# Kernel optimization log

Hardware: AMD Instinct MI355X
Metric: run time of the kernel (lower is better)

The kernel has to match this reference:

```python
import jax, jax.numpy as jnp
import numpy as np

D_MODEL, SEQ, D_HEAD, N_HEAD, D_MLP = 1024, 2048, 64, 16, 4096
BATCH = 2
LN_EPS = 1e-5


def layer_norm(x, gamma, beta):
    mu = jnp.mean(x, axis=-1, keepdims=True)
    var = jnp.mean(jnp.square(x - mu), axis=-1, keepdims=True)
    return (x - mu) * jax.lax.rsqrt(var + LN_EPS) * gamma + beta


def setup_inputs() -> dict:
    key = jax.random.key(0)
    ks = jax.random.split(key, 10)
    s = 1.0 / np.sqrt(D_MODEL)
    x = jax.random.normal(ks[0], (BATCH, SEQ, D_MODEL), dtype=jnp.float32)
    # per-head Q/K/V projections, stacked: [H, d_model, d_head]
    wq = jax.random.uniform(ks[1], (N_HEAD, D_MODEL, D_HEAD), jnp.float32, -s, s)
    wk = jax.random.uniform(ks[2], (N_HEAD, D_MODEL, D_HEAD), jnp.float32, -s, s)
    wv = jax.random.uniform(ks[3], (N_HEAD, D_MODEL, D_HEAD), jnp.float32, -s, s)
    wo = jax.random.uniform(ks[4], (N_HEAD * D_HEAD, D_MODEL), jnp.float32, -s, s)
    sm = 1.0 / np.sqrt(D_MLP)
    w_in = jax.random.uniform(ks[5], (D_MODEL, D_MLP), jnp.float32, -s, s)
    b_in = jax.random.uniform(ks[6], (D_MLP,), jnp.float32, -s, s)
    w_out = jax.random.uniform(ks[7], (D_MLP, D_MODEL), jnp.float32, -sm, sm)
    b_out = jax.random.uniform(ks[8], (D_MODEL,), jnp.float32, -sm, sm)
    g1 = jnp.ones((D_MODEL,), jnp.float32)
    bt1 = jnp.zeros((D_MODEL,), jnp.float32)
    g2 = jnp.ones((D_MODEL,), jnp.float32)
    bt2 = jnp.zeros((D_MODEL,), jnp.float32)
    return {"x": x, "wq": wq, "wk": wk, "wv": wv, "wo": wo,
            "w_in": w_in, "b_in": b_in, "w_out": w_out, "b_out": b_out,
            "g1": g1, "bt1": bt1, "g2": g2, "bt2": bt2}


def reference(x, wq, wk, wv, wo, w_in, b_in, w_out, b_out, g1, bt1, g2, bt2):
    B, S, D = x.shape
    # multi-head attention (all heads batched)
    q = jnp.einsum('bsd,hde->bhse', x, wq)  # [B,H,S,dh]
    k = jnp.einsum('bsd,hde->bhse', x, wk)
    v = jnp.einsum('bsd,hde->bhse', x, wv)
    scores = jnp.einsum('bhie,bhje->bhij', q, k) / np.sqrt(D_HEAD)
    causal = jnp.tril(jnp.ones((S, S), dtype=bool))
    scores = jnp.where(causal, scores, -jnp.inf)
    attn = jax.nn.softmax(scores, axis=-1)
    head_out = jnp.einsum('bhij,bhje->bhie', attn, v)  # [B,H,S,dh]
    # concat heads in order (head 0 first) -> [B,S,H*dh]
    head_out = jnp.transpose(head_out, (0, 2, 1, 3)).reshape(B, S, N_HEAD * D_HEAD)
    x = x + layer_norm(head_out @ wo, g1, bt1)
    mlp = jax.nn.relu(x @ w_in + b_in) @ w_out + b_out
    x = x + layer_norm(mlp, g2, bt2)
    return x
```

## Files before the change

### kernel.cpp

```cpp
#include <hip/hip_runtime.h>
#include <hip/hip_bf16.h>
#include <math.h>

#define DM 1024
#define SEQ 2048
#define DH 64
#define NH 16
#define DMLP 4096
#define BATCH 2
#define ROWS (BATCH*SEQ)

typedef __attribute__((ext_vector_type(4))) float f32x4;
typedef __attribute__((ext_vector_type(8))) short bf16x8;

__device__ __forceinline__ void gl2lds16(const __hip_bfloat16* g, __hip_bfloat16* l) {
  __builtin_amdgcn_global_load_lds(
      (const __attribute__((address_space(1))) void*)g,
      (__attribute__((address_space(3))) void*)l, 16, 0, 0);
}

template<int K, int OUT_BF16, int BIAS, int RELU>
__global__ __launch_bounds__(512) void gemm256(
    const __hip_bfloat16* __restrict__ A,
    const __hip_bfloat16* __restrict__ BT,
    float* __restrict__ Cf,
    __hip_bfloat16* __restrict__ Cb,
    const float* __restrict__ bias,
    int N)
{
  constexpr int NT = K / 64;
  __shared__ __align__(16) __hip_bfloat16 As[2][16384];
  __shared__ __align__(16) __hip_bfloat16 Bs[2][16384];
  const int t    = threadIdx.x;
  const int wave = t >> 6;
  const int lane = t & 63;
  const int col  = lane & 15;
  const int quad = lane >> 4;
  const int m0 = blockIdx.x * 256;
  const int n0 = blockIdx.y * 256;
  const int wm = (wave >> 2) * 128;
  const int wn = (wave & 3) * 64;

  const int tr = t >> 3;
  const int tc = (t & 7) ^ (tr & 7);
  const __hip_bfloat16* gA = A  + (size_t)(m0 + tr) * K + tc * 8;
  const __hip_bfloat16* gB = BT + (size_t)(n0 + tr) * K + tc * 8;

  const int sw  = col & 7;
  const int ao0 = ((quad)     ^ sw) * 8;
  const int ao1 = ((4 + quad) ^ sw) * 8;

  f32x4 acc[8][4] = {};

#define STAGE_A(h, u) do {                                                     \
    gl2lds16(gA + (size_t)(h)*128*K + (u)*64,                                  \
             &As[(u)&1][(h)*8192 + wave*512]);                                 \
    gl2lds16(gA + (size_t)(h)*128*K + (u)*64 + (size_t)64*K,                   \
             &As[(u)&1][(h)*8192 + 4096 + wave*512]);                          \
  } while (0)
#define STAGE_B(h, u) do {                                                     \
    gl2lds16(gB + (size_t)(h)*128*K + (u)*64,                                  \
             &Bs[(u)&1][(h)*8192 + wave*512]);                                 \
    gl2lds16(gB + (size_t)(h)*128*K + (u)*64 + (size_t)64*K,                   \
             &Bs[(u)&1][(h)*8192 + 4096 + wave*512]);                          \
  } while (0)
#define LOAD_A(base) do { _Pragma("unroll")                                    \
    for (int i = 0; i < 4; ++i) {                                              \
      af[i][0] = *(const bf16x8*)(pA + (base) + i*1024 + ao0);                 \
      af[i][1] = *(const bf16x8*)(pA + (base) + i*1024 + ao1);                 \
    } } while (0)
#define LOAD_BX(arr, base) do { _Pragma("unroll")                              \
    for (int j = 0; j < 2; ++j) {                                              \
      arr[j][0] = *(const bf16x8*)(pB + (base) + j*1024 + ao0);                \
      arr[j][1] = *(const bf16x8*)(pB + (base) + j*1024 + ao1);                \
    } } while (0)
#define PHASE_TAIL(MB, NB, BARR) do {                                          \
    asm volatile("s_barrier" ::: "memory");                                    \
    asm volatile("s_waitcnt lgkmcnt(0)" ::: "memory");                         \
    __builtin_amdgcn_s_setprio(1);                                             \
    _Pragma("unroll")                                                          \
    for (int kk = 0; kk < 2; ++kk)                                             \
      _Pragma("unroll")                                                        \
      for (int i = 0; i < 4; ++i)                                              \
        _Pragma("unroll")                                                      \
        for (int j = 0; j < 2; ++j)                                            \
          acc[(MB)+i][(NB)+j] = __builtin_amdgcn_mfma_f32_16x16x32_bf16(       \
              af[i][kk], BARR[j][kk], acc[(MB)+i][(NB)+j], 0, 0, 0);           \
    __builtin_amdgcn_s_setprio(0);                                             \
    asm volatile("s_barrier" ::: "memory");                                    \
  } while (0)

  STAGE_A(0, 0); STAGE_B(0, 0); STAGE_A(1, 0); STAGE_B(1, 0);
  if (NT > 1) {
    STAGE_A(0, 1); STAGE_B(0, 1); STAGE_A(1, 1); STAGE_B(1, 1);
    asm volatile("s_waitcnt vmcnt(8)" ::: "memory");
  } else {
    asm volatile("s_waitcnt vmcnt(0)" ::: "memory");
  }
  asm volatile("s_barrier" ::: "memory");

  #pragma unroll 2
  for (int u = 0; u < NT; ++u) {
    const __hip_bfloat16* pA = As[u & 1] + (wm + col) * 64;
    const __hip_bfloat16* pB = Bs[u & 1] + (wn + col) * 64;
    const bool s2 = (u + 2 < NT);
    bf16x8 af[4][2], bl[2][2], bh[2][2];

    LOAD_A(0);
    LOAD_BX(bl, 0);
    PHASE_TAIL(0, 0, bl);

    LOAD_BX(bh, 2048);
    PHASE_TAIL(0, 2, bh);

    LOAD_A(4096);
    if (s2) { STAGE_B(0, u + 2); STAGE_B(1, u + 2); }
    PHASE_TAIL(4, 2, bh);

    if (s2) {
      STAGE_A(0, u + 2); STAGE_A(1, u + 2);
      asm volatile("s_waitcnt vmcnt(8)" ::: "memory");
    } else {
      asm volatile("s_waitcnt vmcnt(0)" ::: "memory");
    }
    PHASE_TAIL(4, 0, bl);
  }
#undef STAGE_A
#undef STAGE_B
#undef LOAD_A
#undef LOAD_BX
#undef PHASE_TAIL

  #pragma unroll
  for (int mi = 0; mi < 8; ++mi) {
    #pragma unroll
    for (int ni = 0; ni < 4; ++ni) {
      const int cn = n0 + wn + ni*16 + col;
      float bv = 0.f;
      if (BIAS) bv = bias[cn];
      #pragma unroll
      for (int r = 0; r < 4; ++r) {
        const int cm = m0 + wm + mi*16 + quad*4 + r;
        float v = acc[mi][ni][r];
        if (BIAS) v += bv;
        if (RELU) v = fmaxf(v, 0.f);
        if (OUT_BF16) Cb[(size_t)cm * N + cn] = __float2bfloat16(v);
        else          Cf[(size_t)cm * N + cn] = v;
      }
    }
  }
}

template<int TM, int SPLIT, int OUT_BF16, int BIAS, int RELU>
__global__ __launch_bounds__(256) void gemm_bt(
    const __hip_bfloat16* __restrict__ A,
    const __hip_bfloat16* __restrict__ BT,
    float* __restrict__ Cf,
    __hip_bfloat16* __restrict__ Cb,
    const float* __restrict__ bias,
    int M, int N, int K, long long zstride)
{
  constexpr int ASZ = TM*32;
  constexpr int MI  = (TM == 128) ? 4 : 2;
  __shared__ __align__(16) __hip_bfloat16 As[2*ASZ];
  __shared__ __align__(16) __hip_bfloat16 Bs[2*4096];
  const int t    = threadIdx.x;
  const int wave = t >> 6;
  const int lane = t & 63;
  const int col  = lane & 15;
  const int quad = lane >> 4;
  const int m0 = blockIdx.x * TM;
  const int n0 = blockIdx.y * 128;
  const int wm = (wave >> 1) * (TM/2);
  const int wn = (wave & 1) * 64;

  const int Ks = K / SPLIT;
  const int kz = (SPLIT > 1) ? (int)blockIdx.z * Ks : 0;

  const int srow = t >> 2;
  const int scw  = ((t & 3) ^ ((srow >> 1) & 3)) * 8;
  const __hip_bfloat16* gA = A  + (size_t)(m0 + srow) * K + kz + scw;
  const __hip_bfloat16* gB = BT + (size_t)(n0 + srow) * K + kz + scw;
  const size_t rstep = (size_t)64 * K;

  const int scr = (quad ^ ((col >> 1) & 3)) * 8;

  f32x4 acc[MI][4] = {};

#define ISSUE(k0, buf) do {                                            \
    __hip_bfloat16* la = As + (buf)*ASZ  + wave*512;                   \
    __hip_bfloat16* lb = Bs + (buf)*4096 + wave*512;                   \
    gl2lds16(gA + (k0), la);                                           \
    if (TM == 128) gl2lds16(gA + rstep + (k0), la + 2048);             \
    gl2lds16(gB + (k0), lb);                                           \
    gl2lds16(gB + rstep + (k0), lb + 2048);                            \
  } while (0)

  ISSUE(0, 0);
  for (int k0 = 0; k0 < Ks; k0 += 32) {
    const int cur = (k0 >> 5) & 1;
    __syncthreads();
    if (k0 + 32 < Ks) ISSUE(k0 + 32, cur ^ 1);
    const __hip_bfloat16* Ab = As + cur*ASZ;
    const __hip_bfloat16* Bb = Bs + cur*4096;
    bf16x8 af[MI], bf[4];
    #pragma unroll
    for (int i = 0; i < MI; i++)
      af[i] = *(const bf16x8*)&Ab[(wm + i*16 + col)*32 + scr];
    #pragma unroll
    for (int j = 0; j < 4; j++)
      bf[j] = *(const bf16x8*)&Bb[(wn + j*16 + col)*32 + scr];
    #pragma unroll
    for (int i = 0; i < MI; i++)
      #pragma unroll
      for (int j = 0; j < 4; j++)
        acc[i][j] = __builtin_amdgcn_mfma_f32_16x16x32_bf16(af[i], bf[j], acc[i][j], 0, 0, 0);
  }
#undef ISSUE

  float* Cfz = (SPLIT > 1) ? (Cf + (size_t)blockIdx.z * zstride) : Cf;

  #pragma unroll
  for (int i = 0; i < MI; i++) {
    #pragma unroll
    for (int j = 0; j < 4; j++) {
      const int cn = n0 + wn + j*16 + col;
      float bv = 0.f;
      if (BIAS) bv = bias[cn];
      #pragma unroll
      for (int r = 0; r < 4; r++) {
        const int cm = m0 + wm + i*16 + quad*4 + r;
        float v = acc[i][j][r];
        if (BIAS) v += bv;
        if (RELU) v = fmaxf(v, 0.f);
        if (OUT_BF16) Cb[(size_t)cm * N + cn] = __float2bfloat16(v);
        else          Cfz[(size_t)cm * N + cn] = v;
      }
    }
  }
}

__global__ __launch_bounds__(256) void attn_kernel(
    const __hip_bfloat16* __restrict__ qkv,
    const __hip_bfloat16* __restrict__ vt,
    __hip_bfloat16* __restrict__ aout)
{
  __shared__ __align__(16) __hip_bfloat16 Ks[2][64*64];
  __shared__ __align__(16) __hip_bfloat16 Vts[2][64*64];
  __shared__ __align__(16) __hip_bfloat16 Ps[4][16*64];

  const int bh = blockIdx.x, b = bh >> 4, h = bh & 15;
  const int t = threadIdx.x, wave = t >> 6, lane = t & 63;
  const int col = lane & 15, quad = lane >> 4;
  const float SC = 0.125f * 1.44269504f;

  const int r0  = t >> 3;
  const int cs0 = (t & 7) ^ (r0 & 7);
  const __hip_bfloat16* kbase = qkv + (size_t)b*SEQ*3072 + 1024 + h*64;
  const __hip_bfloat16* vbase = vt + (size_t)bh*64*SEQ;

#define AISSUE(j0, buf) do {                                                      \
    gl2lds16(kbase + (size_t)((j0) + r0)*3072      + cs0*8, &Ks[buf][wave*512]);  \
    gl2lds16(kbase + (size_t)((j0) + 32 + r0)*3072 + cs0*8, &Ks[buf][2048 + wave*512]); \
    gl2lds16(vbase + (size_t)r0*SEQ        + (j0) + cs0*8,  &Vts[buf][wave*512]); \
    gl2lds16(vbase + (size_t)(32 + r0)*SEQ + (j0) + cs0*8,  &Vts[buf][2048 + wave*512]); \
  } while (0)

  #pragma unroll 1
  for (int half = 0; half < 2; half++) {
    const int tile = half ? (31 - (int)blockIdx.y) : (int)blockIdx.y;
    const int i0 = tile * 64;
    const int i0w = i0 + wave*16;

    bf16x8 aq[2];
    #pragma unroll
    for (int kk = 0; kk < 2; kk++)
      aq[kk] = *(const bf16x8*)&qkv[((size_t)(b*SEQ + i0w + col))*3072 + h*64 + kk*32 + quad*8];

    f32x4 O[4] = {};
    float lsum[4] = {0.f, 0.f, 0.f, 0.f};

    const int njt = tile + 1;
    __syncthreads();
    AISSUE(0, 0);
    for (int jt = 0; jt < njt; jt++) {
      const int cur = jt & 1;
      const int j0 = jt * 64;
      __syncthreads();
      if (jt + 1 < njt) AISSUE(j0 + 64, cur ^ 1);

      f32x4 S[4] = {};
      #pragma unroll
      for (int kk = 0; kk < 2; kk++) {
        const int sl = ((kk*4 + quad) ^ (col & 7)) * 8;
        #pragma unroll
        for (int jl = 0; jl < 4; jl++) {
          bf16x8 bk = *(const bf16x8*)&Ks[cur][(jl*16 + col)*64 + sl];
          S[jl] = __builtin_amdgcn_mfma_f32_16x16x32_bf16(aq[kk], bk, S[jl], 0, 0, 0);
        }
      }

      const bool diag = (jt == tile);
      #pragma unroll
      for (int r = 0; r < 4; r++) {
        const int row = quad*4 + r;
        const int ig = i0 + wave*16 + row;
        #pragma unroll
        for (int jl = 0; jl < 4; jl++) {
          float p = exp2f(S[jl][r] * SC);
          if (diag && (j0 + jl*16 + col > ig)) p = 0.f;
          lsum[r] += p;
          const int c = jl*2 + (col >> 3);
          Ps[wave][row*64 + (c ^ (row & 7))*8 + (col & 7)] = __float2bfloat16(p);
        }
      }

      #pragma unroll
      for (int kk = 0; kk < 2; kk++) {
        const int sl = ((kk*4 + quad) ^ (col & 7)) * 8;
        bf16x8 ap = *(const bf16x8*)&Ps[wave][col*64 + sl];
        #pragma unroll
        for (int et = 0; et < 4; et++) {
          bf16x8 bv = *(const bf16x8*)&Vts[cur][(et*16 + col)*64 + sl];
          O[et] = __builtin_amdgcn_mfma_f32_16x16x32_bf16(ap, bv, O[et], 0, 0, 0);
        }
      }
    }

    #pragma unroll
    for (int r = 0; r < 4; r++) {
      float s = lsum[r];
      s += __shfl_xor(s, 1);
      s += __shfl_xor(s, 2);
      s += __shfl_xor(s, 4);
      s += __shfl_xor(s, 8);
      const float inv = 1.f / s;
      const int m = b*SEQ + i0w + quad*4 + r;
      #pragma unroll
      for (int et = 0; et < 4; et++)
        aout[(size_t)m*DM + h*64 + et*16 + col] = __float2bfloat16(O[et][r] * inv);
    }
  }
#undef AISSUE
}

__global__ __launch_bounds__(256) void ln_res(
    const float* __restrict__ y0,
    const float* __restrict__ y1,
    const float* __restrict__ bias,
    const float* __restrict__ xres,
    float* __restrict__ xout,
    __hip_bfloat16* __restrict__ bout,
    const float* __restrict__ gamma,
    const float* __restrict__ beta)
{
  const int row = blockIdx.x;
  const int t = threadIdx.x;
  float4 v = ((const float4*)(y0 + (size_t)row*DM))[t];
  if (y1) {
    const float4 w = ((const float4*)(y1 + (size_t)row*DM))[t];
    v.x += w.x; v.y += w.y; v.z += w.z; v.w += w.w;
  }
  if (bias) {
    const float4 w = ((const float4*)bias)[t];
    v.x += w.x; v.y += w.y; v.z += w.z; v.w += w.w;
  }
  float s  = v.x + v.y + v.z + v.w;
  float sq = v.x*v.x + v.y*v.y + v.z*v.z + v.w*v.w;
  #pragma unroll
  for (int off = 32; off > 0; off >>= 1) {
    s  += __shfl_down(s, off);
    sq += __shfl_down(sq, off);
  }
  __shared__ float red[8];
  const int wave = t >> 6, lane = t & 63;
  if (lane == 0) { red[wave] = s; red[4 + wave] = sq; }
  __syncthreads();
  s  = red[0] + red[1] + red[2] + red[3];
  sq = red[4] + red[5] + red[6] + red[7];
  const float mu   = s * (1.f/DM);
  const float var  = sq * (1.f/DM) - mu*mu;
  const float rstd = rsqrtf(var + 1e-5f);
  const float4 g  = ((const float4*)gamma)[t];
  const float4 bt = ((const float4*)beta)[t];
  const float4 xr = ((const float4*)(xres + (size_t)row*DM))[t];
  float4 o;
  o.x = (v.x - mu)*rstd*g.x + bt.x + xr.x;
  o.y = (v.y - mu)*rstd*g.y + bt.y + xr.y;
  o.z = (v.z - mu)*rstd*g.z + bt.z + xr.z;
  o.w = (v.w - mu)*rstd*g.w + bt.w + xr.w;
  ((float4*)(xout + (size_t)row*DM))[t] = o;
  if (bout) {
    __hip_bfloat16* bp = bout + (size_t)row*DM + t*4;
    bp[0] = __float2bfloat16(o.x);
    bp[1] = __float2bfloat16(o.y);
    bp[2] = __float2bfloat16(o.z);
    bp[3] = __float2bfloat16(o.w);
  }
}

__global__ __launch_bounds__(256) void transpose_cvt(
    const float* __restrict__ src, __hip_bfloat16* __restrict__ dst,
    int K, int N, long long sz, long long dz)
{
  __shared__ float tile[32][33];
  const int z = blockIdx.z;
  const int k0 = blockIdx.y * 32, n0 = blockIdx.x * 32;
  const int tx = threadIdx.x & 31, ty = threadIdx.x >> 5;
  const float* s = src + (size_t)z*sz;
  __hip_bfloat16* d = dst + (size_t)z*dz;
  for (int i = ty; i < 32; i += 8)
    tile[i][tx] = s[(size_t)(k0+i)*N + n0 + tx];
  __syncthreads();
  for (int i = ty; i < 32; i += 8)
    d[(size_t)(n0+i)*K + k0 + tx] = __float2bfloat16(tile[tx][i]);
}

__global__ __launch_bounds__(256) void transpose_v(
    const __hip_bfloat16* __restrict__ qkv, __hip_bfloat16* __restrict__ vt)
{
  __shared__ __hip_bfloat16 tile[32][33];
  const int bh = blockIdx.z, b = bh >> 4, h = bh & 15;
  const int s0 = blockIdx.x * 32, e0 = blockIdx.y * 32;
  const int tx = threadIdx.x & 31, ty = threadIdx.x >> 5;
  for (int i = ty; i < 32; i += 8)
    tile[i][tx] = qkv[(size_t)(b*SEQ + s0+i)*3072 + 2048 + h*64 + e0 + tx];
  __syncthreads();
  for (int i = ty; i < 32; i += 8)
    vt[((size_t)bh*64 + e0+i)*SEQ + s0 + tx] = tile[tx][i];
}

__global__ __launch_bounds__(256) void cvt_bf16(
    const float* __restrict__ src, __hip_bfloat16* __restrict__ dst, int n4)
{
  const int i = blockIdx.x*256 + threadIdx.x;
  if (i < n4) {
    const float4 v = ((const float4*)src)[i];
    dst[i*4+0] = __float2bfloat16(v.x);
    dst[i*4+1] = __float2bfloat16(v.y);
    dst[i*4+2] = __float2bfloat16(v.z);
    dst[i*4+3] = __float2bfloat16(v.w);
  }
}

extern "C" void kernel_launch(void* const* d_in, const int* in_sizes, int n_in,
                              void* d_out, int out_size, void* d_ws, size_t ws_size,
                              hipStream_t stream)
{
  const float* x     = (const float*)d_in[0];
  const float* wq    = (const float*)d_in[1];
  const float* wk    = (const float*)d_in[2];
  const float* wv    = (const float*)d_in[3];
  const float* wo    = (const float*)d_in[4];
  const float* w_in  = (const float*)d_in[5];
  const float* b_in  = (const float*)d_in[6];
  const float* w_out = (const float*)d_in[7];
  const float* b_out = (const float*)d_in[8];
  const float* g1    = (const float*)d_in[9];
  const float* bt1   = (const float*)d_in[10];
  const float* g2    = (const float*)d_in[11];
  const float* bt2   = (const float*)d_in[12];
  float* out = (float*)d_out;

  char* ws = (char*)d_ws;
  __hip_bfloat16* xb     = (__hip_bfloat16*)(ws + 0);
  __hip_bfloat16* wqkvT  = (__hip_bfloat16*)(ws + 8388608);
  __hip_bfloat16* woT    = (__hip_bfloat16*)(ws + 14680064);
  __hip_bfloat16* w_inT  = (__hip_bfloat16*)(ws + 16777216);
  __hip_bfloat16* w_outT = (__hip_bfloat16*)(ws + 25165824);
  __hip_bfloat16* qkvb   = (__hip_bfloat16*)(ws + 33554432);
  __hip_bfloat16* vtb    = (__hip_bfloat16*)(ws + 58720256);
  __hip_bfloat16* attn_o = (__hip_bfloat16*)(ws + 67108864);
  float*          P0     = (float*)(ws + 33554432);
  float*          x1     = (float*)(ws + 75497472);
  __hip_bfloat16* x1b    = (__hip_bfloat16*)(ws + 92274688);
  __hip_bfloat16* hbuf   = (__hip_bfloat16*)(ws + 33554432);
  float*          M0     = (float*)(ws + 0);
  float*          M1     = (float*)(ws + 100663296);
  float*          P1     = (float*)(ws + 50331648);

  const long long PROJ_ZS = (long long)ROWS * DM;
  const long long MLP_ZS  = 100663296LL / 4;

  cvt_bf16<<<ROWS*DM/4/256, 256, 0, stream>>>(x, xb, ROWS*DM/4);

  transpose_cvt<<<dim3(2,32,16), 256, 0, stream>>>(wq, wqkvT,             DM, DH, (long long)DM*DH, (long long)DH*DM);
  transpose_cvt<<<dim3(2,32,16), 256, 0, stream>>>(wk, wqkvT + 1024*1024, DM, DH, (long long)DM*DH, (long long)DH*DM);
  transpose_cvt<<<dim3(2,32,16), 256, 0, stream>>>(wv, wqkvT + 2048*1024, DM, DH, (long long)DM*DH, (long long)DH*DM);
  transpose_cvt<<<dim3(32,32,1),  256, 0, stream>>>(wo,    woT,    DM,   DM,   0, 0);
  transpose_cvt<<<dim3(128,32,1), 256, 0, stream>>>(w_in,  w_inT,  DM,   DMLP, 0, 0);
  transpose_cvt<<<dim3(32,128,1), 256, 0, stream>>>(w_out, w_outT, DMLP, DM,   0, 0);

  gemm256<DM,1,0,0><<<dim3(ROWS/256, 3072/256), 512, 0, stream>>>(xb, wqkvT, nullptr, qkvb, nullptr, 3072);
  transpose_v<<<dim3(SEQ/32, 2, BATCH*NH), 256, 0, stream>>>(qkvb, vtb);
  attn_kernel<<<dim3(BATCH*NH, 16), 256, 0, stream>>>(qkvb, vtb, attn_o);
  gemm_bt<64,2,0,0,0><<<dim3(ROWS/64, DM/128, 2), 256, 0, stream>>>(attn_o, woT, P0, nullptr, nullptr, ROWS, DM, DM, PROJ_ZS);
  ln_res<<<ROWS, 256, 0, stream>>>(P0, P1, nullptr, x, x1, x1b, g1, bt1);
  gemm256<DM,1,1,1><<<dim3(ROWS/256, DMLP/256), 512, 0, stream>>>(x1b, w_inT, nullptr, hbuf, b_in, DMLP);
  gemm_bt<64,2,0,0,0><<<dim3(ROWS/64, DM/128, 2), 256, 0, stream>>>(hbuf, w_outT, M0, nullptr, nullptr, ROWS, DM, DMLP, MLP_ZS);
  ln_res<<<ROWS, 256, 0, stream>>>(M0, M1, b_out, x1, out, nullptr, g2, bt2);
}
```

Before: 255.5 us.

## Replace split-K 64x128 GEMM with 256x128 pipelined 512-thread GEMM for projections

Swaps the gemm_bt kernel used for the attention output projection and the MLP down projection for a new 256x128-tile, 8-wave kernel with 64-wide K tiles. It interleaves global-to-LDS loads with MFMA work using explicit waitcnt/barrier control and setprio. The aim is more operand reuse per LDS load and better overlap of memory with compute. The cost is fewer blocks (256 instead of 1024 per launch), so occupancy and load balance across the CUs may suffer.

```diff
diff --git a/kernel.cpp b/kernel.cpp
--- a/kernel.cpp
+++ b/kernel.cpp
@@ -151,90 +151,120 @@
   }
 }
 
-template<int TM, int SPLIT, int OUT_BF16, int BIAS, int RELU>
-__global__ __launch_bounds__(256) void gemm_bt(
+template<int KS>
+__global__ __launch_bounds__(512) void gemm256x128(
     const __hip_bfloat16* __restrict__ A,
     const __hip_bfloat16* __restrict__ BT,
     float* __restrict__ Cf,
-    __hip_bfloat16* __restrict__ Cb,
-    const float* __restrict__ bias,
-    int M, int N, int K, long long zstride)
-{
-  constexpr int ASZ = TM*32;
-  constexpr int MI  = (TM == 128) ? 4 : 2;
-  __shared__ __align__(16) __hip_bfloat16 As[2*ASZ];
-  __shared__ __align__(16) __hip_bfloat16 Bs[2*4096];
+    int N, int K, long long zstride)
+{
+  constexpr int NT = KS / 64;
+  static_assert(NT >= 2, "pipeline needs >=2 K-tiles");
+  __shared__ __align__(16) __hip_bfloat16 As[2][16384];
+  __shared__ __align__(16) __hip_bfloat16 Bs[2][8192];
   const int t    = threadIdx.x;
   const int wave = t >> 6;
   const int lane = t & 63;
   const int col  = lane & 15;
   const int quad = lane >> 4;
-  const int m0 = blockIdx.x * TM;
+  const int m0 = blockIdx.x * 256;
   const int n0 = blockIdx.y * 128;
-  const int wm = (wave >> 1) * (TM/2);
+  const int kz = (int)blockIdx.z * KS;
+  const int wm = (wave >> 1) * 64;
   const int wn = (wave & 1) * 64;
 
-  const int Ks = K / SPLIT;
-  const int kz = (SPLIT > 1) ? (int)blockIdx.z * Ks : 0;
-
-  const int srow = t >> 2;
-  const int scw  = ((t & 3) ^ ((srow >> 1) & 3)) * 8;
-  const __hip_bfloat16* gA = A  + (size_t)(m0 + srow) * K + kz + scw;
-  const __hip_bfloat16* gB = BT + (size_t)(n0 + srow) * K + kz + scw;
-  const size_t rstep = (size_t)64 * K;
-
-  const int scr = (quad ^ ((col >> 1) & 3)) * 8;
-
-  f32x4 acc[MI][4] = {};
-
-#define ISSUE(k0, buf) do {                                            \
-    __hip_bfloat16* la = As + (buf)*ASZ  + wave*512;                   \
-    __hip_bfloat16* lb = Bs + (buf)*4096 + wave*512;                   \
-    gl2lds16(gA + (k0), la);                                           \
-    if (TM == 128) gl2lds16(gA + rstep + (k0), la + 2048);             \
-    gl2lds16(gB + (k0), lb);                                           \
-    gl2lds16(gB + rstep + (k0), lb + 2048);                            \
+  const int tr = t >> 3;
+  const int tc = (t & 7) ^ (tr & 7);
+  const __hip_bfloat16* gA = A  + (size_t)(m0 + tr) * K + kz + tc * 8;
+  const __hip_bfloat16* gB = BT + (size_t)(n0 + tr) * K + kz + tc * 8;
+
+  const int sw  = col & 7;
+  const int ao0 = ((quad)     ^ sw) * 8;
+  const int ao1 = ((4 + quad) ^ sw) * 8;
+
+  f32x4 acc[4][4] = {};
+
+#define SA(u) do { _Pragma("unroll")                                           \
+    for (int q = 0; q < 4; ++q)                                                \
+      gl2lds16(gA + (size_t)(q*64)*K + (u)*64,                                 \
+               &As[(u)&1][q*4096 + wave*512]);                                 \
   } while (0)
-
-  ISSUE(0, 0);
-  for (int k0 = 0; k0 < Ks; k0 += 32) {
-    const int cur = (k0 >> 5) & 1;
-    __syncthreads();
-    if (k0 + 32 < Ks) ISSUE(k0 + 32, cur ^ 1);
-    const __hip_bfloat16* Ab = As + cur*ASZ;
-    const __hip_bfloat16* Bb = Bs + cur*4096;
-    bf16x8 af[MI], bf[4];
-    #pragma unroll
-    for (int i = 0; i < MI; i++)
-      af[i] = *(const bf16x8*)&Ab[(wm + i*16 + col)*32 + scr];
-    #pragma unroll
-    for (int j = 0; j < 4; j++)
-      bf[j] = *(const bf16x8*)&Bb[(wn + j*16 + col)*32 + scr];
-    #pragma unroll
-    for (int i = 0; i < MI; i++)
-      #pragma unroll
-      for (int j = 0; j < 4; j++)
-        acc[i][j] = __builtin_amdgcn_mfma_f32_16x16x32_bf16(af[i], bf[j], acc[i][j], 0, 0, 0);
-  }
-#undef ISSUE
-
-  float* Cfz = (SPLIT > 1) ? (Cf + (size_t)blockIdx.z * zstride) : Cf;
-
+#define SB(u) do { _Pragma("unroll")                                           \
+    for (int q = 0; q < 2; ++q)                                                \
+      gl2lds16(gB + (size_t)(q*64)*K + (u)*64,                                 \
+               &Bs[(u)&1][q*4096 + wave*512]);                                 \
+  } while (0)
+
+  SA(0); SB(0); SA(1);
+
+  #pragma unroll 2
+  for (int v = 0; v < NT; ++v) {
+    const __hip_bfloat16* pA = As[v & 1] + (wm + col) * 64;
+    const __hip_bfloat16* pB = Bs[v & 1] + (wn + col) * 64;
+    bf16x8 af[4][2], bf[4][2];
+
+    if (v + 1 < NT) {
+      SB(v + 1);
+      asm volatile("s_waitcnt vmcnt(6)" ::: "memory");
+    } else {
+      asm volatile("s_waitcnt vmcnt(0)" ::: "memory");
+    }
+    asm volatile("s_barrier" ::: "memory");
+    #pragma unroll
+    for (int i = 0; i < 4; ++i) {
+      af[i][0] = *(const bf16x8*)(pA + i*1024 + ao0);
+      af[i][1] = *(const bf16x8*)(pA + i*1024 + ao1);
+    }
+    #pragma unroll
+    for (int j = 0; j < 2; ++j) {
+      bf[j][0] = *(const bf16x8*)(pB + j*1024 + ao0);
+      bf[j][1] = *(const bf16x8*)(pB + j*1024 + ao1);
+    }
+    asm volatile("s_waitcnt lgkmcnt(0)" ::: "memory");
+    __builtin_amdgcn_s_setprio(1);
+    #pragma unroll
+    for (int kk = 0; kk < 2; ++kk)
+      #pragma unroll
+      for (int i = 0; i < 4; ++i)
+        #pragma unroll
+        for (int j = 0; j < 2; ++j)
+          acc[i][j] = __builtin_amdgcn_mfma_f32_16x16x32_bf16(
+              af[i][kk], bf[j][kk], acc[i][j], 0, 0, 0);
+    __builtin_amdgcn_s_setprio(0);
+    asm volatile("s_barrier" ::: "memory");
+
+    if (v + 2 < NT) SA(v + 2);
+    #pragma unroll
+    for (int j = 2; j < 4; ++j) {
+      bf[j][0] = *(const bf16x8*)(pB + j*1024 + ao0);
+      bf[j][1] = *(const bf16x8*)(pB + j*1024 + ao1);
+    }
+    asm volatile("s_waitcnt lgkmcnt(0)" ::: "memory");
+    __builtin_amdgcn_s_setprio(1);
+    #pragma unroll
+    for (int kk = 0; kk < 2; ++kk)
+      #pragma unroll
+      for (int i = 0; i < 4; ++i)
+        #pragma unroll
+        for (int j = 2; j < 4; ++j)
+          acc[i][j] = __builtin_amdgcn_mfma_f32_16x16x32_bf16(
+              af[i][kk], bf[j][kk], acc[i][j], 0, 0, 0);
+    __builtin_amdgcn_s_setprio(0);
+    asm volatile("s_barrier" ::: "memory");
+  }
+#undef SA
+#undef SB
+
+  float* Co = Cf + (size_t)blockIdx.z * zstride;
   #pragma unroll
-  for (int i = 0; i < MI; i++) {
-    #pragma unroll
-    for (int j = 0; j < 4; j++) {
+  for (int i = 0; i < 4; ++i) {
+    #pragma unroll
+    for (int j = 0; j < 4; ++j) {
       const int cn = n0 + wn + j*16 + col;
-      float bv = 0.f;
-      if (BIAS) bv = bias[cn];
-      #pragma unroll
-      for (int r = 0; r < 4; r++) {
+      #pragma unroll
+      for (int r = 0; r < 4; ++r) {
         const int cm = m0 + wm + i*16 + quad*4 + r;
-        float v = acc[i][j][r];
-        if (BIAS) v += bv;
-        if (RELU) v = fmaxf(v, 0.f);
-        if (OUT_BF16) Cb[(size_t)cm * N + cn] = __float2bfloat16(v);
-        else          Cfz[(size_t)cm * N + cn] = v;
+        Co[(size_t)cm * N + cn] = acc[i][j][r];
       }
     }
   }
@@ -494,9 +524,9 @@
   gemm256<DM,1,0,0><<<dim3(ROWS/256, 3072/256), 512, 0, stream>>>(xb, wqkvT, nullptr, qkvb, nullptr, 3072);
   transpose_v<<<dim3(SEQ/32, 2, BATCH*NH), 256, 0, stream>>>(qkvb, vtb);
   attn_kernel<<<dim3(BATCH*NH, 16), 256, 0, stream>>>(qkvb, vtb, attn_o);
-  gemm_bt<64,2,0,0,0><<<dim3(ROWS/64, DM/128, 2), 256, 0, stream>>>(attn_o, woT, P0, nullptr, nullptr, ROWS, DM, DM, PROJ_ZS);
+  gemm256x128<512><<<dim3(ROWS/256, DM/128, 2), 512, 0, stream>>>(attn_o, woT, P0, DM, DM, PROJ_ZS);
   ln_res<<<ROWS, 256, 0, stream>>>(P0, P1, nullptr, x, x1, x1b, g1, bt1);
   gemm256<DM,1,1,1><<<dim3(ROWS/256, DMLP/256), 512, 0, stream>>>(x1b, w_inT, nullptr, hbuf, b_in, DMLP);
-  gemm_bt<64,2,0,0,0><<<dim3(ROWS/64, DM/128, 2), 256, 0, stream>>>(hbuf, w_outT, M0, nullptr, nullptr, ROWS, DM, DMLP, MLP_ZS);
+  gemm256x128<2048><<<dim3(ROWS/256, DM/128, 2), 512, 0, stream>>>(hbuf, w_outT, M0, DM, DMLP, MLP_ZS);
   ln_res<<<ROWS, 256, 0, stream>>>(M0, M1, b_out, x1, out, nullptr, g2, bt2);
 }
```

New measurement: 233.7 us. 8.5% less time.
